# Kernel tuning notes

Measured on AMD Instinct MI355X. Metric: run time of the kernel, lower is better.

The kernel has to match this reference:

```python
import jax, jax.numpy as jnp
import numpy as np

E, C, H, I = 8, 4096, 1024, 4096

def setup_inputs() -> dict:
    key = jax.random.key(0)
    k_x, k_g, k_u, k_d = jax.random.split(key, 4)
    scale_h = 1.0 / np.sqrt(H)
    scale_i = 1.0 / np.sqrt(I)
    return {
        "x_routed": jax.random.normal(k_x, (E, C, H), dtype=jnp.float32),
        "W_gate": jax.random.normal(k_g, (E, H, I), dtype=jnp.float32) * scale_h,
        "W_up": jax.random.normal(k_u, (E, H, I), dtype=jnp.float32) * scale_h,
        "W_down": jax.random.normal(k_d, (E, I, H), dtype=jnp.float32) * scale_i,
    }

def reference(x_routed, W_gate, W_up, W_down):
    # Per-expert SwiGLU MLP, batched over the expert axis as a grouped GEMM.
    # gate = silu(x @ Wg); up = x @ Wu; out = (gate * up) @ Wd
    gate = jax.nn.silu(jnp.einsum("ech,ehi->eci", x_routed, W_gate))
    up = jnp.einsum("ech,ehi->eci", x_routed, W_up)
    out = jnp.einsum("eci,eih->ech", gate * up, W_down)
    return out
```

## Files before the change

kernel.cpp:

```cpp
#include <hip/hip_runtime.h>
#include <hip/hip_bf16.h>
#include <stdint.h>
#include <stddef.h>

#define E_ 8
#define C_ 4096
#define H_ 1024
#define I_ 4096

typedef short s16;
typedef __attribute__((ext_vector_type(8))) short short8;
typedef __attribute__((ext_vector_type(4))) short short4v;
typedef __attribute__((ext_vector_type(4))) float f32x4;
typedef __attribute__((ext_vector_type(4))) float float4v;

__device__ __forceinline__ s16 f2bf(float f) {
  union { __hip_bfloat16 h; s16 s; } u;
  u.h = __float2bfloat16(f);
  return u.s;
}

__device__ __forceinline__ void gload16(const void* gsrc, void* ldst) {
  __builtin_amdgcn_global_load_lds(
      (const __attribute__((address_space(1))) void*)gsrc,
      (__attribute__((address_space(3))) void*)ldst, 16, 0, 0);
}

__global__ __launch_bounds__(256) void prep_kernel(
    const float* __restrict__ x, const float* __restrict__ Wg,
    const float* __restrict__ Wu, const float* __restrict__ Wd,
    s16* __restrict__ xb, s16* __restrict__ Wgu, s16* __restrict__ WdT)
{
  __shared__ float tile[64][65];
  const int t = threadIdx.x;
  const int z = blockIdx.z;
  const size_t e = blockIdx.y;

  if (z == 0) {
    size_t base = e * (size_t)C_ * H_ + ((size_t)blockIdx.x * 256 + t) * 16;
    for (int j = 0; j < 16; j += 8) {
      float4v v0 = *(const float4v*)(x + base + j);
      float4v v1 = *(const float4v*)(x + base + j + 4);
      s16 o[8];
      o[0] = f2bf(v0[0]); o[1] = f2bf(v0[1]); o[2] = f2bf(v0[2]); o[3] = f2bf(v0[3]);
      o[4] = f2bf(v1[0]); o[5] = f2bf(v1[1]); o[6] = f2bf(v1[2]); o[7] = f2bf(v1[3]);
      *(short8*)(xb + base + j) = *(short8*)o;
    }
    return;
  }

  const float* src; int Cc;
  if (z == 1)      { src = Wg + e * (size_t)H_ * I_; Cc = I_; }
  else if (z == 2) { src = Wu + e * (size_t)H_ * I_; Cc = I_; }
  else             { src = Wd + e * (size_t)H_ * I_; Cc = H_; }

  const int tpr  = Cc >> 6;
  const int trow = blockIdx.x / tpr;
  const int tcol = blockIdx.x % tpr;

  const int c = t & 63, rq = t >> 6;
  for (int i = 0; i < 16; ++i) {
    int r = rq * 16 + i;
    tile[r][c] = src[(size_t)(trow * 64 + r) * Cc + tcol * 64 + c];
  }
  __syncthreads();

  const int ro = t >> 2, cb = (t & 3) * 16;
  s16 o[16];
  for (int j = 0; j < 16; ++j) o[j] = f2bf(tile[cb + j][ro]);

  const int i0 = tcol * 64 + ro;
  s16* op;
  if (z == 3) {
    op = WdT + e * (size_t)H_ * I_ + (size_t)i0 * I_ + trow * 64 + cb;
  } else {
    int grow = ((i0 & ~15) << 1) + (i0 & 15) + ((z == 2) ? 16 : 0);
    op = Wgu + e * (size_t)2 * I_ * H_ + (size_t)grow * H_ + trow * 64 + cb;
  }
  *(short8*)op       = *(short8*)&o[0];
  *(short8*)(op + 8) = *(short8*)&o[8];
}

#define MFMA16(MH, A0, A1, A2, A3)                                                            \
  acc[(MH)*4+0][0] = __builtin_amdgcn_mfma_f32_16x16x32_bf16(bf[0], A0, acc[(MH)*4+0][0],0,0,0); \
  acc[(MH)*4+0][1] = __builtin_amdgcn_mfma_f32_16x16x32_bf16(bf[1], A0, acc[(MH)*4+0][1],0,0,0); \
  acc[(MH)*4+0][2] = __builtin_amdgcn_mfma_f32_16x16x32_bf16(bf[2], A0, acc[(MH)*4+0][2],0,0,0); \
  acc[(MH)*4+0][3] = __builtin_amdgcn_mfma_f32_16x16x32_bf16(bf[3], A0, acc[(MH)*4+0][3],0,0,0); \
  acc[(MH)*4+1][0] = __builtin_amdgcn_mfma_f32_16x16x32_bf16(bf[0], A1, acc[(MH)*4+1][0],0,0,0); \
  acc[(MH)*4+1][1] = __builtin_amdgcn_mfma_f32_16x16x32_bf16(bf[1], A1, acc[(MH)*4+1][1],0,0,0); \
  acc[(MH)*4+1][2] = __builtin_amdgcn_mfma_f32_16x16x32_bf16(bf[2], A1, acc[(MH)*4+1][2],0,0,0); \
  acc[(MH)*4+1][3] = __builtin_amdgcn_mfma_f32_16x16x32_bf16(bf[3], A1, acc[(MH)*4+1][3],0,0,0); \
  acc[(MH)*4+2][0] = __builtin_amdgcn_mfma_f32_16x16x32_bf16(bf[0], A2, acc[(MH)*4+2][0],0,0,0); \
  acc[(MH)*4+2][1] = __builtin_amdgcn_mfma_f32_16x16x32_bf16(bf[1], A2, acc[(MH)*4+2][1],0,0,0); \
  acc[(MH)*4+2][2] = __builtin_amdgcn_mfma_f32_16x16x32_bf16(bf[2], A2, acc[(MH)*4+2][2],0,0,0); \
  acc[(MH)*4+2][3] = __builtin_amdgcn_mfma_f32_16x16x32_bf16(bf[3], A2, acc[(MH)*4+2][3],0,0,0); \
  acc[(MH)*4+3][0] = __builtin_amdgcn_mfma_f32_16x16x32_bf16(bf[0], A3, acc[(MH)*4+3][0],0,0,0); \
  acc[(MH)*4+3][1] = __builtin_amdgcn_mfma_f32_16x16x32_bf16(bf[1], A3, acc[(MH)*4+3][1],0,0,0); \
  acc[(MH)*4+3][2] = __builtin_amdgcn_mfma_f32_16x16x32_bf16(bf[2], A3, acc[(MH)*4+3][2],0,0,0); \
  acc[(MH)*4+3][3] = __builtin_amdgcn_mfma_f32_16x16x32_bf16(bf[3], A3, acc[(MH)*4+3][3],0,0,0);

#define VMW4 asm volatile("s_waitcnt vmcnt(4)" ::: "memory");

#define LDAF(B, MH, M, CX) \
  (*(const short8*)(shm + (B)*16384 + ((wm + (MH)*64 + (M)*16 + lr) << 6) + (CX)))
#define LDBF(B, N, CX) \
  (*(const short8*)(shm + 32768 + (B)*16384 + ((wn + (N)*16 + lr) << 6) + (CX)))

#define PHASE(B, MH, CX, RDB, STMT, WV)                                      \
  {                                                                          \
    short8 af0 = LDAF(B, MH, 0, CX);                                         \
    short8 af1 = LDAF(B, MH, 1, CX);                                         \
    short8 af2 = LDAF(B, MH, 2, CX);                                         \
    short8 af3 = LDAF(B, MH, 3, CX);                                         \
    if (RDB) {                                                               \
      bf[0] = LDBF(B, 0, CX); bf[1] = LDBF(B, 1, CX);                        \
      bf[2] = LDBF(B, 2, CX); bf[3] = LDBF(B, 3, CX);                        \
    }                                                                        \
    STMT                                                                     \
    __builtin_amdgcn_sched_barrier(0);                                       \
    __builtin_amdgcn_s_barrier();                                            \
    asm volatile("s_waitcnt lgkmcnt(0)" ::: "memory");                       \
    __builtin_amdgcn_sched_barrier(0);                                       \
    __builtin_amdgcn_s_setprio(1);                                           \
    MFMA16(MH, af0, af1, af2, af3)                                           \
    __builtin_amdgcn_s_setprio(0);                                           \
    __builtin_amdgcn_sched_barrier(0);                                       \
    WV                                                                       \
    __builtin_amdgcn_s_barrier();                                            \
  }

__global__ __launch_bounds__(512, 2) void gemm_gu(
    const s16* __restrict__ Abase, const s16* __restrict__ Bbase,
    s16* __restrict__ HOut)
{
  constexpr int K   = H_;
  constexpr int NB  = 2 * I_;
  constexpr int NT  = K / 64;
  constexpr int NTL = 4;
  constexpr int VT  = NTL * NT;

  __shared__ s16 shm[65536];

  const int tid  = threadIdx.x;
  const int wave = tid >> 6, lane = tid & 63;
  const int e    = blockIdx.z;

  const int bid = blockIdx.x;
  const int bnc = bid & 7;
  const int bm  = bid >> 3;

  const s16* A  = Abase + (size_t)e * C_ * K + (size_t)bm * 256 * K;
  const s16* B0 = Bbase + (size_t)e * NB * K + (size_t)bnc * NTL * 256 * K;

  const int wm  = (wave >> 2) * 128;
  const int wn  = (wave & 3) * 64;
  const int lr  = lane & 15;
  const int lkb = (lane >> 4) * 8;
  const int xr  = (lr & 7) << 3;
  const int cx0 = lkb ^ xr;
  const int cx1 = (32 + lkb) ^ xr;

  const int srow = tid >> 3;
  const int scol = ((tid & 7) ^ (srow & 7)) * 8;
  const size_t stoff = (size_t)srow * K + scol;
  const int sdst = wave * 512;

  auto stageA = [&](int vt, int b) {
    const int kt = vt & (NT - 1);
    #pragma unroll
    for (int h = 0; h < 2; ++h)
      #pragma unroll
      for (int ll = 0; ll < 2; ++ll)
        gload16(A + (size_t)(h * 128 + ll * 64) * K + (size_t)kt * 64 + stoff,
                shm + b * 16384 + h * 8192 + ll * 4096 + sdst);
  };
  auto stageB = [&](int vt, int b) {
    const int kt = vt & (NT - 1);
    const s16* Bp = B0 + (size_t)(vt >> 4) * (256 * K);
    #pragma unroll
    for (int h = 0; h < 2; ++h)
      #pragma unroll
      for (int ll = 0; ll < 2; ++ll)
        gload16(Bp + (size_t)(h * 128 + ll * 64) * K + (size_t)kt * 64 + stoff,
                shm + 32768 + b * 16384 + h * 8192 + ll * 4096 + sdst);
  };

  f32x4 acc[8][4];
  #pragma unroll
  for (int m = 0; m < 8; ++m)
    #pragma unroll
    for (int n = 0; n < 4; ++n) acc[m][n] = (f32x4){0.f, 0.f, 0.f, 0.f};

  stageB(0, 0);
  stageA(0, 0);
  stageB(1, 1);
  VMW4
  __builtin_amdgcn_sched_barrier(0);
  __builtin_amdgcn_s_barrier();

  short8 bf[4];
  const int lcc = (lane >> 4) * 4;
  s16* Hp = HOut + (size_t)e * C_ * I_;

  for (int j = 0; j < NTL; ++j) {
    for (int ii = 0; ii < NT / 2; ++ii) {
      const int v  = j * NT + 2 * ii;
      const int t1 = v + 1;
      const int t2 = (v + 2 < VT) ? v + 2 : VT - 1;
      const int t3 = (v + 3 < VT) ? v + 3 : VT - 1;
      PHASE(0, 0, cx0, 1, { stageA(t1, 1); }, )
      PHASE(0, 1, cx0, 0, {}, )
      PHASE(0, 0, cx1, 1, {}, )
      PHASE(0, 1, cx1, 0, { stageB(t2, 0); }, VMW4)
      PHASE(1, 0, cx0, 1, { stageA(t2, 0); }, )
      PHASE(1, 1, cx0, 0, {}, )
      PHASE(1, 0, cx1, 1, {}, )
      PHASE(1, 1, cx1, 0, { stageB(t3, 1); }, VMW4)
    }

    {
      const int bn = bnc * NTL + j;
      const int ibase = bn * 128 + (wn >> 1);
      #pragma unroll
      for (int m = 0; m < 8; ++m) {
        const int row = bm * 256 + wm + m * 16 + lr;
        #pragma unroll
        for (int p = 0; p < 2; ++p) {
          const int col = ibase + p * 16 + lcc;
          s16 o4[4];
          #pragma unroll
          for (int q = 0; q < 4; ++q) {
            float g = acc[m][2 * p][q], u = acc[m][2 * p + 1][q];
            float sg = 1.0f / (1.0f + __expf(-g));
            o4[q] = f2bf(g * sg * u);
          }
          *(short4v*)(Hp + (size_t)row * I_ + col) = *(short4v*)o4;
        }
      }
      if (j + 1 < NTL) {
        #pragma unroll
        for (int m = 0; m < 8; ++m)
          #pragma unroll
          for (int n = 0; n < 4; ++n) acc[m][n] = (f32x4){0.f, 0.f, 0.f, 0.f};
      }
    }
  }
}

__global__ __launch_bounds__(512, 2) void gemm_dn(
    const s16* __restrict__ Abase, const s16* __restrict__ Bbase,
    float* __restrict__ FOut)
{
  constexpr int K  = I_;
  constexpr int NB = H_;
  constexpr int NT = K / 64;
  constexpr int TN = NB / 256;
  constexpr int TM = C_ / 256;
  constexpr int NWG = TM * TN;

  __shared__ s16 shm[65536];

  const int tid  = threadIdx.x;
  const int wave = tid >> 6, lane = tid & 63;
  const int e    = blockIdx.z;

  const int bid = blockIdx.x;
  const int swz = (bid & 7) * (NWG / 8) + (bid >> 3);
  const int bm = swz / TN, bn = swz % TN;

  const s16* A = Abase + (size_t)e * C_ * K + (size_t)bm * 256 * K;
  const s16* B = Bbase + (size_t)e * NB * K + (size_t)bn * 256 * K;

  const int wm  = (wave >> 2) * 128;
  const int wn  = (wave & 3) * 64;
  const int lr  = lane & 15;
  const int lkb = (lane >> 4) * 8;
  const int xr  = (lr & 7) << 3;
  const int cx0 = lkb ^ xr;
  const int cx1 = (32 + lkb) ^ xr;

  const int srow = tid >> 3;
  const int scol = ((tid & 7) ^ (srow & 7)) * 8;
  const size_t stoff = (size_t)srow * K + scol;
  const int sdst = wave * 512;

  auto stageA = [&](int kt, int b) {
    #pragma unroll
    for (int h = 0; h < 2; ++h)
      #pragma unroll
      for (int ll = 0; ll < 2; ++ll)
        gload16(A + (size_t)(h * 128 + ll * 64) * K + (size_t)kt * 64 + stoff,
                shm + b * 16384 + h * 8192 + ll * 4096 + sdst);
  };
  auto stageB = [&](int kt, int b) {
    #pragma unroll
    for (int h = 0; h < 2; ++h)
      #pragma unroll
      for (int ll = 0; ll < 2; ++ll)
        gload16(B + (size_t)(h * 128 + ll * 64) * K + (size_t)kt * 64 + stoff,
                shm + 32768 + b * 16384 + h * 8192 + ll * 4096 + sdst);
  };

  f32x4 acc[8][4];
  #pragma unroll
  for (int m = 0; m < 8; ++m)
    #pragma unroll
    for (int n = 0; n < 4; ++n) acc[m][n] = (f32x4){0.f, 0.f, 0.f, 0.f};

  stageB(0, 0);
  stageA(0, 0);
  stageB(1, 1);
  VMW4
  __builtin_amdgcn_sched_barrier(0);
  __builtin_amdgcn_s_barrier();

  short8 bf[4];
  for (int i = 0; i < NT / 2; ++i) {
    const int t1 = 2 * i + 1;
    const int t2 = (2 * i + 2 < NT) ? (2 * i + 2) : (NT - 1);
    const int t3 = (2 * i + 3 < NT) ? (2 * i + 3) : (NT - 1);
    PHASE(0, 0, cx0, 1, { stageA(t1, 1); }, )
    PHASE(0, 1, cx0, 0, {}, )
    PHASE(0, 0, cx1, 1, {}, )
    PHASE(0, 1, cx1, 0, { stageB(t2, 0); }, VMW4)
    PHASE(1, 0, cx0, 1, { stageA(t2, 0); }, )
    PHASE(1, 1, cx0, 0, {}, )
    PHASE(1, 0, cx1, 1, {}, )
    PHASE(1, 1, cx1, 0, { stageB(t3, 1); }, VMW4)
  }

  const int lcc = (lane >> 4) * 4;
  float* Op = FOut + (size_t)e * C_ * H_;
  #pragma unroll
  for (int m = 0; m < 8; ++m) {
    const int row = bm * 256 + wm + m * 16 + lr;
    #pragma unroll
    for (int n = 0; n < 4; ++n) {
      const int col = bn * 256 + wn + n * 16 + lcc;
      *(float4v*)(Op + (size_t)row * H_ + col) = acc[m][n];
    }
  }
}

extern "C" void kernel_launch(void* const* d_in, const int* in_sizes, int n_in,
                              void* d_out, int out_size, void* d_ws, size_t ws_size,
                              hipStream_t stream) {
  const float* x  = (const float*)d_in[0];
  const float* Wg = (const float*)d_in[1];
  const float* Wu = (const float*)d_in[2];
  const float* Wd = (const float*)d_in[3];
  float* out = (float*)d_out;

  const size_t szX  = (size_t)C_ * H_;
  const size_t szGU = (size_t)2 * I_ * H_;
  const size_t szWd = (size_t)H_ * I_;
  const size_t szH  = (size_t)C_ * I_;

  const size_t needFull = 2 * E_ * (szX + szGU + szWd + szH);

  constexpr int GU_BLK = (C_ / 256) * ((2 * I_ / 256) / 4);
  constexpr int DN_BLK = (C_ / 256) * (H_ / 256);

  if (ws_size >= needFull) {
    s16* xb  = (s16*)d_ws;
    s16* Wgu = xb  + E_ * szX;
    s16* WdT = Wgu + E_ * szGU;
    s16* hbf = WdT + E_ * szWd;

    prep_kernel<<<dim3(1024, E_, 4), 256, 0, stream>>>(
        x, Wg, Wu, Wd, xb, Wgu, WdT);
    gemm_gu<<<dim3(GU_BLK, 1, E_), 512, 0, stream>>>(
        xb, Wgu, hbf);
    gemm_dn<<<dim3(DN_BLK, 1, E_), 512, 0, stream>>>(
        hbf, WdT, out);
  } else {
    s16* xb  = (s16*)d_ws;
    s16* Wgu = xb  + szX;
    s16* WdT = Wgu + szGU;
    s16* hbf = WdT + szWd;

    for (int e = 0; e < E_; ++e) {
      prep_kernel<<<dim3(1024, 1, 4), 256, 0, stream>>>(
          x + e * szX, Wg + e * szWd, Wu + e * szWd, Wd + e * szWd,
          xb, Wgu, WdT);
      gemm_gu<<<dim3(GU_BLK, 1, 1), 512, 0, stream>>>(
          xb, Wgu, hbf);
      gemm_dn<<<dim3(DN_BLK, 1, 1), 512, 0, stream>>>(
          hbf, WdT, out + e * szX);
    }
  }
}
```

Before: 961.2 us.

## Split gate/up GEMM into one 256-column tile per block with XCD-aware mapping

```diff
diff --git a/kernel.cpp b/kernel.cpp
--- a/kernel.cpp
+++ b/kernel.cpp
@@ -133,11 +133,9 @@
     const s16* __restrict__ Abase, const s16* __restrict__ Bbase,
     s16* __restrict__ HOut)
 {
-  constexpr int K   = H_;
-  constexpr int NB  = 2 * I_;
-  constexpr int NT  = K / 64;
-  constexpr int NTL = 4;
-  constexpr int VT  = NTL * NT;
+  constexpr int K  = H_;
+  constexpr int NB = 2 * I_;
+  constexpr int NT = K / 64;
 
   __shared__ s16 shm[65536];
 
@@ -146,127 +144,10 @@
   const int e    = blockIdx.z;
 
   const int bid = blockIdx.x;
-  const int bnc = bid & 7;
-  const int bm  = bid >> 3;
-
-  const s16* A  = Abase + (size_t)e * C_ * K + (size_t)bm * 256 * K;
-  const s16* B0 = Bbase + (size_t)e * NB * K + (size_t)bnc * NTL * 256 * K;
-
-  const int wm  = (wave >> 2) * 128;
-  const int wn  = (wave & 3) * 64;
-  const int lr  = lane & 15;
-  const int lkb = (lane >> 4) * 8;
-  const int xr  = (lr & 7) << 3;
-  const int cx0 = lkb ^ xr;
-  const int cx1 = (32 + lkb) ^ xr;
-
-  const int srow = tid >> 3;
-  const int scol = ((tid & 7) ^ (srow & 7)) * 8;
-  const size_t stoff = (size_t)srow * K + scol;
-  const int sdst = wave * 512;
-
-  auto stageA = [&](int vt, int b) {
-    const int kt = vt & (NT - 1);
-    #pragma unroll
-    for (int h = 0; h < 2; ++h)
-      #pragma unroll
-      for (int ll = 0; ll < 2; ++ll)
-        gload16(A + (size_t)(h * 128 + ll * 64) * K + (size_t)kt * 64 + stoff,
-                shm + b * 16384 + h * 8192 + ll * 4096 + sdst);
-  };
-  auto stageB = [&](int vt, int b) {
-    const int kt = vt & (NT - 1);
-    const s16* Bp = B0 + (size_t)(vt >> 4) * (256 * K);
-    #pragma unroll
-    for (int h = 0; h < 2; ++h)
-      #pragma unroll
-      for (int ll = 0; ll < 2; ++ll)
-        gload16(Bp + (size_t)(h * 128 + ll * 64) * K + (size_t)kt * 64 + stoff,
-                shm + 32768 + b * 16384 + h * 8192 + ll * 4096 + sdst);
-  };
-
-  f32x4 acc[8][4];
-  #pragma unroll
-  for (int m = 0; m < 8; ++m)
-    #pragma unroll
-    for (int n = 0; n < 4; ++n) acc[m][n] = (f32x4){0.f, 0.f, 0.f, 0.f};
-
-  stageB(0, 0);
-  stageA(0, 0);
-  stageB(1, 1);
-  VMW4
-  __builtin_amdgcn_sched_barrier(0);
-  __builtin_amdgcn_s_barrier();
-
-  short8 bf[4];
-  const int lcc = (lane >> 4) * 4;
-  s16* Hp = HOut + (size_t)e * C_ * I_;
-
-  for (int j = 0; j < NTL; ++j) {
-    for (int ii = 0; ii < NT / 2; ++ii) {
-      const int v  = j * NT + 2 * ii;
-      const int t1 = v + 1;
-      const int t2 = (v + 2 < VT) ? v + 2 : VT - 1;
-      const int t3 = (v + 3 < VT) ? v + 3 : VT - 1;
-      PHASE(0, 0, cx0, 1, { stageA(t1, 1); }, )
-      PHASE(0, 1, cx0, 0, {}, )
-      PHASE(0, 0, cx1, 1, {}, )
-      PHASE(0, 1, cx1, 0, { stageB(t2, 0); }, VMW4)
-      PHASE(1, 0, cx0, 1, { stageA(t2, 0); }, )
-      PHASE(1, 1, cx0, 0, {}, )
-      PHASE(1, 0, cx1, 1, {}, )
-      PHASE(1, 1, cx1, 0, { stageB(t3, 1); }, VMW4)
-    }
-
-    {
-      const int bn = bnc * NTL + j;
-      const int ibase = bn * 128 + (wn >> 1);
-      #pragma unroll
-      for (int m = 0; m < 8; ++m) {
-        const int row = bm * 256 + wm + m * 16 + lr;
-        #pragma unroll
-        for (int p = 0; p < 2; ++p) {
-          const int col = ibase + p * 16 + lcc;
-          s16 o4[4];
-          #pragma unroll
-          for (int q = 0; q < 4; ++q) {
-            float g = acc[m][2 * p][q], u = acc[m][2 * p + 1][q];
-            float sg = 1.0f / (1.0f + __expf(-g));
-            o4[q] = f2bf(g * sg * u);
-          }
-          *(short4v*)(Hp + (size_t)row * I_ + col) = *(short4v*)o4;
-        }
-      }
-      if (j + 1 < NTL) {
-        #pragma unroll
-        for (int m = 0; m < 8; ++m)
-          #pragma unroll
-          for (int n = 0; n < 4; ++n) acc[m][n] = (f32x4){0.f, 0.f, 0.f, 0.f};
-      }
-    }
-  }
-}
-
-__global__ __launch_bounds__(512, 2) void gemm_dn(
-    const s16* __restrict__ Abase, const s16* __restrict__ Bbase,
-    float* __restrict__ FOut)
-{
-  constexpr int K  = I_;
-  constexpr int NB = H_;
-  constexpr int NT = K / 64;
-  constexpr int TN = NB / 256;
-  constexpr int TM = C_ / 256;
-  constexpr int NWG = TM * TN;
-
-  __shared__ s16 shm[65536];
-
-  const int tid  = threadIdx.x;
-  const int wave = tid >> 6, lane = tid & 63;
-  const int e    = blockIdx.z;
-
-  const int bid = blockIdx.x;
-  const int swz = (bid & 7) * (NWG / 8) + (bid >> 3);
-  const int bm = swz / TN, bn = swz % TN;
+  const int xcd = bid & 7;
+  const int idx = bid >> 3;
+  const int bn = (xcd & 3) * 8 + (idx & 7);
+  const int bm = (xcd >> 2) * 8 + (idx >> 3);
 
   const s16* A = Abase + (size_t)e * C_ * K + (size_t)bm * 256 * K;
   const s16* B = Bbase + (size_t)e * NB * K + (size_t)bn * 256 * K;
@@ -330,6 +211,109 @@
   }
 
   const int lcc = (lane >> 4) * 4;
+  s16* Hp = HOut + (size_t)e * C_ * I_;
+  const int ibase = bn * 128 + (wn >> 1);
+  #pragma unroll
+  for (int m = 0; m < 8; ++m) {
+    const int row = bm * 256 + wm + m * 16 + lr;
+    #pragma unroll
+    for (int p = 0; p < 2; ++p) {
+      const int col = ibase + p * 16 + lcc;
+      s16 o4[4];
+      #pragma unroll
+      for (int q = 0; q < 4; ++q) {
+        float g = acc[m][2 * p][q], u = acc[m][2 * p + 1][q];
+        float sg = 1.0f / (1.0f + __expf(-g));
+        o4[q] = f2bf(g * sg * u);
+      }
+      *(short4v*)(Hp + (size_t)row * I_ + col) = *(short4v*)o4;
+    }
+  }
+}
+
+__global__ __launch_bounds__(512, 2) void gemm_dn(
+    const s16* __restrict__ Abase, const s16* __restrict__ Bbase,
+    float* __restrict__ FOut)
+{
+  constexpr int K  = I_;
+  constexpr int NB = H_;
+  constexpr int NT = K / 64;
+  constexpr int TN = NB / 256;
+  constexpr int TM = C_ / 256;
+  constexpr int NWG = TM * TN;
+
+  __shared__ s16 shm[65536];
+
+  const int tid  = threadIdx.x;
+  const int wave = tid >> 6, lane = tid & 63;
+  const int e    = blockIdx.z;
+
+  const int bid = blockIdx.x;
+  const int swz = (bid & 7) * (NWG / 8) + (bid >> 3);
+  const int bm = swz / TN, bn = swz % TN;
+
+  const s16* A = Abase + (size_t)e * C_ * K + (size_t)bm * 256 * K;
+  const s16* B = Bbase + (size_t)e * NB * K + (size_t)bn * 256 * K;
+
+  const int wm  = (wave >> 2) * 128;
+  const int wn  = (wave & 3) * 64;
+  const int lr  = lane & 15;
+  const int lkb = (lane >> 4) * 8;
+  const int xr  = (lr & 7) << 3;
+  const int cx0 = lkb ^ xr;
+  const int cx1 = (32 + lkb) ^ xr;
+
+  const int srow = tid >> 3;
+  const int scol = ((tid & 7) ^ (srow & 7)) * 8;
+  const size_t stoff = (size_t)srow * K + scol;
+  const int sdst = wave * 512;
+
+  auto stageA = [&](int kt, int b) {
+    #pragma unroll
+    for (int h = 0; h < 2; ++h)
+      #pragma unroll
+      for (int ll = 0; ll < 2; ++ll)
+        gload16(A + (size_t)(h * 128 + ll * 64) * K + (size_t)kt * 64 + stoff,
+                shm + b * 16384 + h * 8192 + ll * 4096 + sdst);
+  };
+  auto stageB = [&](int kt, int b) {
+    #pragma unroll
+    for (int h = 0; h < 2; ++h)
+      #pragma unroll
+      for (int ll = 0; ll < 2; ++ll)
+        gload16(B + (size_t)(h * 128 + ll * 64) * K + (size_t)kt * 64 + stoff,
+                shm + 32768 + b * 16384 + h * 8192 + ll * 4096 + sdst);
+  };
+
+  f32x4 acc[8][4];
+  #pragma unroll
+  for (int m = 0; m < 8; ++m)
+    #pragma unroll
+    for (int n = 0; n < 4; ++n) acc[m][n] = (f32x4){0.f, 0.f, 0.f, 0.f};
+
+  stageB(0, 0);
+  stageA(0, 0);
+  stageB(1, 1);
+  VMW4
+  __builtin_amdgcn_sched_barrier(0);
+  __builtin_amdgcn_s_barrier();
+
+  short8 bf[4];
+  for (int i = 0; i < NT / 2; ++i) {
+    const int t1 = 2 * i + 1;
+    const int t2 = (2 * i + 2 < NT) ? (2 * i + 2) : (NT - 1);
+    const int t3 = (2 * i + 3 < NT) ? (2 * i + 3) : (NT - 1);
+    PHASE(0, 0, cx0, 1, { stageA(t1, 1); }, )
+    PHASE(0, 1, cx0, 0, {}, )
+    PHASE(0, 0, cx1, 1, {}, )
+    PHASE(0, 1, cx1, 0, { stageB(t2, 0); }, VMW4)
+    PHASE(1, 0, cx0, 1, { stageA(t2, 0); }, )
+    PHASE(1, 1, cx0, 0, {}, )
+    PHASE(1, 0, cx1, 1, {}, )
+    PHASE(1, 1, cx1, 0, { stageB(t3, 1); }, VMW4)
+  }
+
+  const int lcc = (lane >> 4) * 4;
   float* Op = FOut + (size_t)e * C_ * H_;
   #pragma unroll
   for (int m = 0; m < 8; ++m) {
@@ -358,7 +342,7 @@
 
   const size_t needFull = 2 * E_ * (szX + szGU + szWd + szH);
 
-  constexpr int GU_BLK = (C_ / 256) * ((2 * I_ / 256) / 4);
+  constexpr int GU_BLK = (C_ / 256) * (2 * I_ / 256);
   constexpr int DN_BLK = (C_ / 256) * (H_ / 256);
 
   if (ws_size >= needFull) {
```

New measurement: 958.3 us. Within noise of the previous version (-0.3%).
